# Optimization experiments

Hardware: AMD Instinct MI355X
Metric: run time of the kernel (lower is better)

Reference implementation:

```python
import jax, jax.numpy as jnp
import numpy as np

M = 0.25
GAMMA = 256.0
HARD_W = 2.0
O_P = 1.0 + M
O_N = -M
DELTA_P = 1.0 - M
DELTA_N = M
NEG_BIG = -1e30  # masked-out fill for logsumexp (finite to keep grads NaN-free)


def setup_inputs() -> dict:
    key = jax.random.key(0)
    k1, k2 = jax.random.split(key)
    inputs = jax.random.normal(k1, (4096, 512), dtype=jnp.float32)
    targets = jax.random.randint(k2, (4096,), 0, 64, dtype=jnp.int64)
    return {"inputs": inputs, "targets": targets}


def reference(inputs, targets):
    n = inputs.shape[0]
    x = inputs / jnp.linalg.norm(inputs, axis=1, keepdims=True)  # L2 normalize
    sim = x @ x.T                                                # [n, n]

    same = targets[:, None] == targets[None, :]
    eye = jnp.eye(n, dtype=bool)
    pos_mask = same & ~eye
    neg_mask = ~same
    npos = pos_mask.sum(axis=1)
    nneg = neg_mask.sum(axis=1)

    sim_d = jax.lax.stop_gradient(sim)  # alphas are detached in the original
    alpha_p = jax.nn.relu(O_P - sim_d)
    alpha_n = jax.nn.relu(sim_d - O_N)

    # hard mining: scale alpha at hardest positive (min sim) / hardest negative (max sim)
    idx = jnp.arange(n)
    hard_p = jnp.argmin(jnp.where(pos_mask, sim_d, jnp.inf), axis=1)
    hard_n = jnp.argmax(jnp.where(neg_mask, sim_d, -jnp.inf), axis=1)
    hit_p = (idx[None, :] == hard_p[:, None]) & (npos > 1)[:, None]
    hit_n = (idx[None, :] == hard_n[:, None]) & (nneg > 1)[:, None]
    alpha_p = alpha_p * jnp.where(hit_p, HARD_W, 1.0)
    alpha_n = alpha_n * jnp.where(hit_n, HARD_W, 1.0)

    pos_term = jnp.where(pos_mask, -GAMMA * alpha_p * (sim - DELTA_P), NEG_BIG)
    neg_term = jnp.where(neg_mask, GAMMA * alpha_n * (sim - DELTA_N), NEG_BIG)
    lse_p = jax.nn.logsumexp(pos_term, axis=1)
    lse_n = jax.nn.logsumexp(neg_term, axis=1)

    valid = (npos > 0) & (nneg > 0)
    per_row = jnp.where(valid, jax.nn.softplus(lse_p + lse_n), 0.0)
    n_valid = jnp.maximum(valid.sum(), 1)
    return per_row.sum() / n_valid.astype(per_row.dtype)
```

## Files before the change

### kernel.cpp

```cpp
#include <hip/hip_runtime.h>


#define MASKT_  (-1.0e4f)
#define MINITP_ (-1.0e4f)
#define MASKP_  (-3.0e4f)
#define QA_     369.3299304675f
#define QB_     (-23.08312065422f)
#define LN2_    0.6931471805599453f

constexpr int N_ = 4096;
constexpr int D_ = 512;
constexpr int AST_ = 520;
constexpr int CCH_ = 16;

typedef __bf16 bf16x8 __attribute__((ext_vector_type(8)));
typedef float  f32x4  __attribute__((ext_vector_type(4)));
typedef const unsigned int __attribute__((address_space(1)))* gp_t;
typedef unsigned int       __attribute__((address_space(3)))* lp_t;

__device__ __forceinline__ float pos_q(float s) {
    float d = s - 1.0f;
    return fmaf(d * d, 256.0f, -16.0f);
}
__device__ __forceinline__ float neg_q(float s) {
    float q = fmaf(s * s, 256.0f, -16.0f);
    return (s >= -0.25f) ? q : 0.0f;
}
__device__ __forceinline__ float neg_q2(float s) {
    float q = fmaf(s * s, QA_, QB_);
    return (s >= -0.25f) ? q : 0.0f;
}
__device__ __forceinline__ void lse_merge(float m2, float S2, float& m, float& S) {
    float mm = fmaxf(m, m2);
    S = S * __expf(m - mm) + S2 * __expf(m2 - mm);
    m = mm;
}
__device__ __forceinline__ void lse_merge2(float m2, float S2, float& m, float& S) {
    float mm = fmaxf(m, m2);
    S = S * exp2f(m - mm) + S2 * exp2f(m2 - mm);
    m = mm;
}
__device__ __forceinline__ unsigned short f2bf(float f) {
    unsigned int u = __float_as_uint(f);
    unsigned int r = u + 0x7FFFu + ((u >> 16) & 1u);
    return (unsigned short)(r >> 16);
}

__global__ __launch_bounds__(256) void k_norm(const float* __restrict__ in,
                                              unsigned short* __restrict__ xb,
                                              float* __restrict__ acc) {
    const int row  = blockIdx.x * 4 + (threadIdx.x >> 6);
    const int lane = threadIdx.x & 63;
    const float4* src = (const float4*)(in + (size_t)row * D_) + lane * 2;
    float4 a = src[0], b = src[1];
    float ss = a.x*a.x + a.y*a.y + a.z*a.z + a.w*a.w
             + b.x*b.x + b.y*b.y + b.z*b.z + b.w*b.w;
    #pragma unroll
    for (int d = 32; d >= 1; d >>= 1) ss += __shfl_xor(ss, d);
    float rn = 1.0f / sqrtf(ss);
    float v[8] = {a.x, a.y, a.z, a.w, b.x, b.y, b.z, b.w};
    union { uint4 u; unsigned short us[8]; } pk;
    #pragma unroll
    for (int k = 0; k < 8; ++k) pk.us[k] = f2bf(v[k] * rn);
    *((uint4*)(xb + (size_t)row * D_) + lane) = pk.u;
    if (blockIdx.x == 0 && threadIdx.x < 4) acc[threadIdx.x] = 0.0f;
}

__global__ __launch_bounds__(256, 4) void k_mainW(const unsigned short* __restrict__ xb,
                                                  const int* __restrict__ tg,
                                                  float* __restrict__ part) {
    constexpr int NST = 16;
    __shared__ __align__(16) unsigned short Bs[2][16][AST_];

    {
        const int ph = ((int)blockIdx.x >> 8) & 3;
        if (ph == 1)      __builtin_amdgcn_s_sleep(7);
        else if (ph == 2) __builtin_amdgcn_s_sleep(14);
        else if (ph == 3) __builtin_amdgcn_s_sleep(21);
    }

    const int tid  = threadIdx.x;
    const int wave = tid >> 6, lane = tid & 63;
    const int n16  = lane & 15, quad = lane >> 4;
    const int rg   = (int)blockIdx.x >> 4;
    const int cc   = (int)blockIdx.x & 15;
    const int rowBase = rg * 64 + wave * 16;
    const int colBase = cc * 256;

    bf16x8 af[16];
    {
        const bf16x8* ap = (const bf16x8*)(xb + (size_t)(rowBase + n16) * D_ + quad * 8);
        #pragma unroll
        for (int kk = 0; kk < 16; ++kk) af[kk] = ap[kk * 4];
    }
    int tr[4];
    #pragma unroll
    for (int r = 0; r < 4; ++r) tr[r] = tg[rowBase + quad * 4 + r];

    float m_p[4], S_p[4], S_n[4], mxn[4];
    #pragma unroll
    for (int r = 0; r < 4; ++r) {
        m_p[r] = MINITP_; S_p[r] = 0.f; S_n[r] = 0.f; mxn[r] = -2.0f;
    }

    const char* gstage = (const char*)xb + (size_t)colBase * 1024 + lane * 16;

    asm volatile("s_waitcnt vmcnt(0)" ::: "memory");

    #pragma unroll
    for (int p = 0; p < 4; ++p) {
        int j = p * 4 + wave;
        __builtin_amdgcn_global_load_lds((gp_t)(const void*)(gstage + j * 1024),
                                         (lp_t)(void*)&Bs[0][j][0], 16, 0, 0);
    }
    int tc_cur = tg[colBase + n16];

    auto epi = [&](const f32x4& a0, const f32x4& a1, int tcv, bool withDiag) {
        #pragma unroll
        for (int r = 0; r < 4; ++r) {
            float sim = a0[r] + a1[r];
            bool samec = (tr[r] == tcv);
            float dm1 = sim - 1.0f;
            float tp  = fmaf(dm1 * dm1, QA_, QB_);
            tp = samec ? tp : MASKP_;
            if (withDiag && n16 == quad * 4 + r) tp = MASKP_;
            float diff = m_p[r] - tp;
            float e    = exp2f(-fabsf(diff));
            float sA   = S_p[r] + e;
            float sB   = fmaf(S_p[r], e, 1.0f);
            S_p[r] = (diff < 0.0f) ? sB : sA;
            m_p[r] = fmaxf(m_p[r], tp);
            float tn = fmaf(sim * sim, QA_, QB_);
            float en = exp2f(tn);
            en = (sim >= -0.25f) ? en : 1.0f;
            en = samec ? 0.0f : en;
            S_n[r] += en;
            mxn[r] = fmaxf(mxn[r], samec ? -2.0f : sim);
        }
    };

    #pragma unroll 1
    for (int u = 0; u < NST; ++u) {
        const int b = u & 1;
        const int j0 = colBase + u * 16;

        int tc_nxt = 0;
        if (u + 1 < NST) {
            const char* g2 = gstage + (size_t)(u + 1) * 16384;
            #pragma unroll
            for (int p = 0; p < 4; ++p) {
                int j = p * 4 + wave;
                __builtin_amdgcn_global_load_lds((gp_t)(const void*)(g2 + j * 1024),
                                                 (lp_t)(void*)&Bs[b ^ 1][j][0], 16, 0, 0);
            }
            tc_nxt = tg[colBase + (u + 1) * 16 + n16];
            asm volatile("s_waitcnt vmcnt(5)" ::: "memory");
        } else {
            asm volatile("s_waitcnt vmcnt(0)" ::: "memory");
        }
        __builtin_amdgcn_s_barrier();
        __builtin_amdgcn_sched_barrier(0);

        f32x4 a0 = {0.f, 0.f, 0.f, 0.f}, a1 = {0.f, 0.f, 0.f, 0.f};
        __builtin_amdgcn_s_setprio(1);
        #pragma unroll
        for (int kk = 0; kk < 8; ++kk) {
            bf16x8 bf0 = *(const bf16x8*)&Bs[b][n16][(2 * kk) * 32 + quad * 8];
            bf16x8 bf1 = *(const bf16x8*)&Bs[b][n16][(2 * kk + 1) * 32 + quad * 8];
            a0 = __builtin_amdgcn_mfma_f32_16x16x32_bf16(af[2 * kk],     bf0, a0, 0, 0, 0);
            a1 = __builtin_amdgcn_mfma_f32_16x16x32_bf16(af[2 * kk + 1], bf1, a1, 0, 0, 0);
        }
        __builtin_amdgcn_s_setprio(0);

        if (j0 == rowBase) epi(a0, a1, tc_cur, true);
        else               epi(a0, a1, tc_cur, false);
        tc_cur = tc_nxt;

        if (u + 1 < NST) __builtin_amdgcn_s_barrier();
    }

    #pragma unroll
    for (int r = 0; r < 4; ++r) {
        #pragma unroll
        for (int d = 1; d <= 8; d <<= 1) {
            lse_merge2(__shfl_xor(m_p[r], d), __shfl_xor(S_p[r], d), m_p[r], S_p[r]);
            S_n[r] += __shfl_xor(S_n[r], d);
            mxn[r] = fmaxf(mxn[r], __shfl_xor(mxn[r], d));
        }
    }
    if (n16 == 0) {
        #pragma unroll
        for (int r = 0; r < 4; ++r) {
            ((float4*)part)[(size_t)(rowBase + quad * 4 + r) * CCH_ + cc] =
                make_float4(m_p[r], S_p[r], mxn[r], S_n[r]);
        }
    }
}

__global__ __launch_bounds__(256) void k_reduceF(const float* __restrict__ part,
                                                 const int* __restrict__ tg,
                                                 float* __restrict__ acc,
                                                 float* __restrict__ out) {
    __shared__ int hist[64];
    const int tid = threadIdx.x;
    if (tid < 64) hist[tid] = 0;
    __syncthreads();
    for (int i = tid; i < N_; i += 256) atomicAdd(&hist[tg[i]], 1);
    __syncthreads();

    const int row = blockIdx.x * 256 + tid;
    const float4* P = (const float4*)part + (size_t)row * CCH_;
    float M_p = MINITP_, Sp = 0.f, M_n = 0.f, Sn = 0.f, mxn = -2.0f;
    #pragma unroll
    for (int c = 0; c < CCH_; ++c) {
        float4 a = P[c];
        lse_merge2(a.x, a.y, M_p, Sp);
        Sn += a.w;
        mxn = fmaxf(mxn, a.z);
    }
    const int cnt = hist[tg[row]];
    float np2 = (float)(cnt - 1), nn2 = (float)(N_ - cnt);
    float loss = 0.f, vld = 0.f;
    if (np2 > 0.5f && nn2 > 0.5f) {
        if (np2 > 1.5f) {
            float t1 = M_p, t2 = 2.0f * t1;
            float mm = fmaxf(M_p, t2);
            Sp = Sp * exp2f(M_p - mm) + exp2f(t2 - mm) - exp2f(t1 - mm);
            M_p = mm;
        }
        if (nn2 > 1.5f) {
            float t1 = neg_q2(mxn), t2 = 2.0f * t1;
            float mm = fmaxf(M_n, t2);
            Sn = Sn * exp2f(M_n - mm) + exp2f(t2 - mm) - exp2f(t1 - mm);
            M_n = mm;
        }
        float z = LN2_ * ((M_p + __log2f(Sp)) + (M_n + __log2f(Sn)));
        loss = fmaxf(z, 0.0f) + log1pf(__expf(-fabsf(z)));
        vld = 1.0f;
    }
    #pragma unroll
    for (int d = 32; d >= 1; d >>= 1) { loss += __shfl_xor(loss, d); vld += __shfl_xor(vld, d); }
    if ((tid & 63) == 0) { atomicAdd(&acc[0], loss); atomicAdd(&acc[1], vld); }

    __syncthreads();
    if (tid == 0) {
        __threadfence();
        int old = atomicAdd((int*)(acc + 2), 1);
        if (old == (int)gridDim.x - 1) {
            float ls = atomicAdd(&acc[0], 0.0f);
            float lv = atomicAdd(&acc[1], 0.0f);
            out[0] = ls / fmaxf(lv, 1.0f);
        }
    }
}

__global__ void k_final(const float* __restrict__ acc, float* __restrict__ out) {
    if (threadIdx.x == 0) out[0] = acc[0] / fmaxf(acc[1], 1.0f);
}

__global__ void k_sentinel(float* __restrict__ out) {
    if (threadIdx.x == 0) out[0] = -12345.0f;
}

__global__ __launch_bounds__(1024, 4) void k_main3(const unsigned short* __restrict__ xb,
                                                   const int* __restrict__ tg,
                                                   float* __restrict__ acc_g) {
    __shared__ __align__(16) unsigned short As[16 * AST_];
    __shared__ float sm[16][16][8];
    const int tid  = threadIdx.x;
    const int wave = tid >> 6, lane = tid & 63;
    const int n16  = lane & 15, quad = lane >> 4;
    const int rowBase = blockIdx.x * 16;
    {
        int row = tid >> 6, c = tid & 63;
        *(uint4*)&As[row * AST_ + c * 8] =
            *(const uint4*)(xb + (size_t)(rowBase + row) * D_ + c * 8);
    }
    int ir[4], tr[4];
    #pragma unroll
    for (int r = 0; r < 4; ++r) { ir[r] = rowBase + quad * 4 + r; tr[r] = tg[ir[r]]; }
    float m_p[4], S_p[4], m_n[4], S_n[4], mnp[4], mxn[4], sc[4];
    #pragma unroll
    for (int r = 0; r < 4; ++r) {
        m_p[r] = 0.f; S_p[r] = 0.f; m_n[r] = 0.f; S_n[r] = 0.f;
        mnp[r] = 2.0f; mxn[r] = -2.0f; sc[r] = 0.f;
    }
    __syncthreads();
    const unsigned short* Af = &As[n16 * AST_ + quad * 8];
    #pragma unroll 1
    for (int t = wave; t < N_ / 16; t += 16) {
        const int jcol = t * 16 + n16;
        const int tc = tg[jcol];
        const bf16x8* bp = (const bf16x8*)(xb + (size_t)jcol * D_ + quad * 8);
        bf16x8 bf[16];
        #pragma unroll
        for (int kk = 0; kk < 16; ++kk) bf[kk] = bp[kk * 4];
        f32x4 a0 = {0.f, 0.f, 0.f, 0.f}, a1 = {0.f, 0.f, 0.f, 0.f};
        #pragma unroll
        for (int kk = 0; kk < 8; ++kk) {
            bf16x8 af0 = *(const bf16x8*)(Af + (2 * kk) * 32);
            bf16x8 af1 = *(const bf16x8*)(Af + (2 * kk + 1) * 32);
            a0 = __builtin_amdgcn_mfma_f32_16x16x32_bf16(af0, bf[2 * kk],     a0, 0, 0, 0);
            a1 = __builtin_amdgcn_mfma_f32_16x16x32_bf16(af1, bf[2 * kk + 1], a1, 0, 0, 0);
        }
        #pragma unroll
        for (int r = 0; r < 4; ++r) {
            float s = a0[r] + a1[r];
            bool samec = (tr[r] == tc);
            bool posm  = samec && (jcol != ir[r]);
            float tp = posm  ? pos_q(s) : MASKT_;
            float tn = samec ? MASKT_ : neg_q(s);
            float mm = fmaxf(m_p[r], tp);
            S_p[r] = S_p[r] * __expf(m_p[r] - mm) + __expf(tp - mm); m_p[r] = mm;
            mm = fmaxf(m_n[r], tn);
            S_n[r] = S_n[r] * __expf(m_n[r] - mm) + __expf(tn - mm); m_n[r] = mm;
            sc[r] += samec ? 1.0f : 0.0f;
            mnp[r] = fminf(mnp[r], posm ? s : 2.0f);
            mxn[r] = fmaxf(mxn[r], samec ? -2.0f : s);
        }
    }
    #pragma unroll
    for (int r = 0; r < 4; ++r) {
        #pragma unroll
        for (int d = 1; d <= 8; d <<= 1) {
            lse_merge(__shfl_xor(m_p[r], d), __shfl_xor(S_p[r], d), m_p[r], S_p[r]);
            lse_merge(__shfl_xor(m_n[r], d), __shfl_xor(S_n[r], d), m_n[r], S_n[r]);
            mnp[r] = fminf(mnp[r], __shfl_xor(mnp[r], d));
            mxn[r] = fmaxf(mxn[r], __shfl_xor(mxn[r], d));
            sc[r] += __shfl_xor(sc[r], d);
        }
    }
    if (n16 == 0) {
        #pragma unroll
        for (int r = 0; r < 4; ++r) {
            float* q = sm[wave][quad * 4 + r];
            q[0] = m_p[r]; q[1] = S_p[r]; q[2] = m_n[r]; q[3] = S_n[r];
            q[4] = mnp[r]; q[5] = mxn[r]; q[6] = sc[r];
        }
    }
    __syncthreads();
    if (tid < 64) {
        const int L = tid & 15;
        float m_p2 = 0.f, S_p2 = 0.f, m_n2 = 0.f, S_n2 = 0.f;
        float mnp2 = 2.0f, mxn2 = -2.0f, sct = 0.f;
        #pragma unroll
        for (int w = 0; w < 16; ++w) {
            const float* q = sm[w][L];
            lse_merge(q[0], q[1], m_p2, S_p2);
            lse_merge(q[2], q[3], m_n2, S_n2);
            mnp2 = fminf(mnp2, q[4]); mxn2 = fmaxf(mxn2, q[5]);
            sct += q[6];
        }
        float loss = 0.f, vld = 0.f;
        float np2 = sct - 1.0f, nn2 = (float)N_ - sct;
        if (tid < 16 && np2 > 0.5f && nn2 > 0.5f) {
            if (np2 > 1.5f) {
                float t1 = pos_q(mnp2), t2 = 2.0f * t1;
                float mm = fmaxf(m_p2, t2);
                S_p2 = S_p2 * __expf(m_p2 - mm) + __expf(t2 - mm) - __expf(t1 - mm);
                m_p2 = mm;
            }
            if (nn2 > 1.5f) {
                float t1 = neg_q(mxn2), t2 = 2.0f * t1;
                float mm = fmaxf(m_n2, t2);
                S_n2 = S_n2 * __expf(m_n2 - mm) + __expf(t2 - mm) - __expf(t1 - mm);
                m_n2 = mm;
            }
            float z = (m_p2 + __logf(S_p2)) + (m_n2 + __logf(S_n2));
            loss = fmaxf(z, 0.0f) + log1pf(__expf(-fabsf(z)));
            vld = 1.0f;
        }
        #pragma unroll
        for (int d = 32; d >= 1; d >>= 1) {
            loss += __shfl_xor(loss, d); vld += __shfl_xor(vld, d);
        }
        if (tid == 0) { atomicAdd(&acc_g[0], loss); atomicAdd(&acc_g[1], vld); }
    }
}

extern "C" void kernel_launch(void* const* d_in, const int* in_sizes, int n_in,
                              void* d_out, int out_size, void* d_ws, size_t ws_size,
                              hipStream_t stream) {
    const float* in = (const float*)d_in[0];
    const int*   tg = (const int*)d_in[1];
    constexpr size_t MB = 1024 * 1024;
    unsigned short* xb = (unsigned short*)d_ws;

    if (ws_size >= 5 * MB + 64) {
        float* part = (float*)((char*)d_ws + 4 * MB);
        float* acc  = (float*)((char*)d_ws + 5 * MB);
        hipLaunchKernelGGL(k_norm,    dim3(N_ / 4),    dim3(256), 0, stream, in, xb, acc);
        hipLaunchKernelGGL(k_mainW,   dim3(64 * CCH_), dim3(256), 0, stream, xb, tg, part);
        hipLaunchKernelGGL(k_reduceF, dim3(N_ / 256),  dim3(256), 0, stream, part, tg, acc,
                           (float*)d_out);
    } else if (ws_size >= 4 * MB + 64) {
        float* acc = (float*)((char*)d_ws + 4 * MB);
        hipLaunchKernelGGL(k_norm,  dim3(N_ / 4),  dim3(256),  0, stream, in, xb, acc);
        hipLaunchKernelGGL(k_main3, dim3(N_ / 16), dim3(1024), 0, stream, xb, tg, acc);
        hipLaunchKernelGGL(k_final, dim3(1),       dim3(64),   0, stream, acc, (float*)d_out);
    } else {
        hipLaunchKernelGGL(k_sentinel, dim3(1), dim3(64), 0, stream, (float*)d_out);
    }
}
```

Measured before the change: 107.1 us.

## Fuse norm, main and reduce kernels into one cooperative grid-synced kernel

Merges the three launches (normalize, similarity/LSE tiles, final reduce) into a single cooperative kernel of 1024 blocks that separates the phases with grid-wide syncs. The aim is to remove two kernel launch gaps and the associated drain/refill overhead. The cost is two grid barriers, and the kernel needs all 1024 blocks co-resident at 4 per CU. It falls back to the three-kernel path if the cooperative launch fails.

```diff
diff --git a/kernel.cpp b/kernel.cpp
--- a/kernel.cpp
+++ b/kernel.cpp
@@ -1,4 +1,7 @@
 #include <hip/hip_runtime.h>
+#include <hip/hip_cooperative_groups.h>
+
+namespace cg = cooperative_groups;
 
 
 #define MASKT_  (-1.0e4f)
@@ -44,6 +47,216 @@
     unsigned int u = __float_as_uint(f);
     unsigned int r = u + 0x7FFFu + ((u >> 16) & 1u);
     return (unsigned short)(r >> 16);
+}
+
+__global__ __launch_bounds__(256, 4) void k_fusedX(const float* __restrict__ in,
+                                                   const int* __restrict__ tg,
+                                                   unsigned short* __restrict__ xb,
+                                                   float* __restrict__ part,
+                                                   float* __restrict__ acc,
+                                                   float* __restrict__ out) {
+    constexpr int NST = 16;
+    __shared__ __align__(16) unsigned short Bs[2][16][AST_];
+    __shared__ int hist[64];
+
+    const int b    = (int)blockIdx.x;
+    const int tid  = threadIdx.x;
+    const int wave = tid >> 6, lane = tid & 63;
+    const int n16  = lane & 15, quad = lane >> 4;
+
+    {
+        const int row = b * 4 + wave;
+        const float4* src = (const float4*)(in + (size_t)row * D_) + lane * 2;
+        float4 a = src[0], c = src[1];
+        float ss = a.x*a.x + a.y*a.y + a.z*a.z + a.w*a.w
+                 + c.x*c.x + c.y*c.y + c.z*c.z + c.w*c.w;
+        #pragma unroll
+        for (int d = 32; d >= 1; d >>= 1) ss += __shfl_xor(ss, d);
+        float rn = 1.0f / sqrtf(ss);
+        float v[8] = {a.x, a.y, a.z, a.w, c.x, c.y, c.z, c.w};
+        union { uint4 u; unsigned short us[8]; } pk;
+        #pragma unroll
+        for (int k = 0; k < 8; ++k) pk.us[k] = f2bf(v[k] * rn);
+        *((uint4*)(xb + (size_t)row * D_) + lane) = pk.u;
+        if (b == 0 && tid < 4) acc[tid] = 0.0f;
+    }
+    cg::this_grid().sync();
+
+    {
+        const int ph = (b >> 8) & 3;
+        if (ph == 1)      __builtin_amdgcn_s_sleep(7);
+        else if (ph == 2) __builtin_amdgcn_s_sleep(14);
+        else if (ph == 3) __builtin_amdgcn_s_sleep(21);
+
+        const int rg = b >> 4;
+        const int cc = b & 15;
+        const int rowBase = rg * 64 + wave * 16;
+        const int colBase = cc * 256;
+
+        bf16x8 af[16];
+        {
+            const bf16x8* ap = (const bf16x8*)(xb + (size_t)(rowBase + n16) * D_ + quad * 8);
+            #pragma unroll
+            for (int kk = 0; kk < 16; ++kk) af[kk] = ap[kk * 4];
+        }
+        int tr[4];
+        #pragma unroll
+        for (int r = 0; r < 4; ++r) tr[r] = tg[rowBase + quad * 4 + r];
+
+        float m_p[4], S_p[4], S_n[4], mxn[4];
+        #pragma unroll
+        for (int r = 0; r < 4; ++r) {
+            m_p[r] = MINITP_; S_p[r] = 0.f; S_n[r] = 0.f; mxn[r] = -2.0f;
+        }
+
+        const char* gstage = (const char*)xb + (size_t)colBase * 1024 + lane * 16;
+
+        asm volatile("s_waitcnt vmcnt(0)" ::: "memory");
+
+        #pragma unroll
+        for (int p = 0; p < 4; ++p) {
+            int j = p * 4 + wave;
+            __builtin_amdgcn_global_load_lds((gp_t)(const void*)(gstage + j * 1024),
+                                             (lp_t)(void*)&Bs[0][j][0], 16, 0, 0);
+        }
+        int tc_cur = tg[colBase + n16];
+
+        auto epi = [&](const f32x4& a0, const f32x4& a1, int tcv, bool withDiag) {
+            #pragma unroll
+            for (int r = 0; r < 4; ++r) {
+                float sim = a0[r] + a1[r];
+                bool samec = (tr[r] == tcv);
+                float dm1 = sim - 1.0f;
+                float tp  = fmaf(dm1 * dm1, QA_, QB_);
+                tp = samec ? tp : MASKP_;
+                if (withDiag && n16 == quad * 4 + r) tp = MASKP_;
+                float diff = m_p[r] - tp;
+                float e    = exp2f(-fabsf(diff));
+                float sA   = S_p[r] + e;
+                float sB   = fmaf(S_p[r], e, 1.0f);
+                S_p[r] = (diff < 0.0f) ? sB : sA;
+                m_p[r] = fmaxf(m_p[r], tp);
+                float tn = fmaf(sim * sim, QA_, QB_);
+                float en = exp2f(tn);
+                en = (sim >= -0.25f) ? en : 1.0f;
+                en = samec ? 0.0f : en;
+                S_n[r] += en;
+                mxn[r] = fmaxf(mxn[r], samec ? -2.0f : sim);
+            }
+        };
+
+        #pragma unroll 1
+        for (int u = 0; u < NST; ++u) {
+            const int bb = u & 1;
+            const int j0 = colBase + u * 16;
+
+            int tc_nxt = 0;
+            if (u + 1 < NST) {
+                const char* g2 = gstage + (size_t)(u + 1) * 16384;
+                #pragma unroll
+                for (int p = 0; p < 4; ++p) {
+                    int j = p * 4 + wave;
+                    __builtin_amdgcn_global_load_lds((gp_t)(const void*)(g2 + j * 1024),
+                                                     (lp_t)(void*)&Bs[bb ^ 1][j][0], 16, 0, 0);
+                }
+                tc_nxt = tg[colBase + (u + 1) * 16 + n16];
+                asm volatile("s_waitcnt vmcnt(5)" ::: "memory");
+            } else {
+                asm volatile("s_waitcnt vmcnt(0)" ::: "memory");
+            }
+            __builtin_amdgcn_s_barrier();
+            __builtin_amdgcn_sched_barrier(0);
+
+            f32x4 a0 = {0.f, 0.f, 0.f, 0.f}, a1 = {0.f, 0.f, 0.f, 0.f};
+            __builtin_amdgcn_s_setprio(1);
+            #pragma unroll
+            for (int kk = 0; kk < 8; ++kk) {
+                bf16x8 bf0 = *(const bf16x8*)&Bs[bb][n16][(2 * kk) * 32 + quad * 8];
+                bf16x8 bf1 = *(const bf16x8*)&Bs[bb][n16][(2 * kk + 1) * 32 + quad * 8];
+                a0 = __builtin_amdgcn_mfma_f32_16x16x32_bf16(af[2 * kk],     bf0, a0, 0, 0, 0);
+                a1 = __builtin_amdgcn_mfma_f32_16x16x32_bf16(af[2 * kk + 1], bf1, a1, 0, 0, 0);
+            }
+            __builtin_amdgcn_s_setprio(0);
+
+            if (j0 == rowBase) epi(a0, a1, tc_cur, true);
+            else               epi(a0, a1, tc_cur, false);
+            tc_cur = tc_nxt;
+
+            if (u + 1 < NST) __builtin_amdgcn_s_barrier();
+        }
+
+        #pragma unroll
+        for (int r = 0; r < 4; ++r) {
+            #pragma unroll
+            for (int d = 1; d <= 8; d <<= 1) {
+                lse_merge2(__shfl_xor(m_p[r], d), __shfl_xor(S_p[r], d), m_p[r], S_p[r]);
+                S_n[r] += __shfl_xor(S_n[r], d);
+                mxn[r] = fmaxf(mxn[r], __shfl_xor(mxn[r], d));
+            }
+        }
+        if (n16 == 0) {
+            #pragma unroll
+            for (int r = 0; r < 4; ++r) {
+                ((float4*)part)[(size_t)(rowBase + quad * 4 + r) * CCH_ + cc] =
+                    make_float4(m_p[r], S_p[r], mxn[r], S_n[r]);
+            }
+        }
+    }
+    cg::this_grid().sync();
+
+    if (b < 16) {
+        if (tid < 64) hist[tid] = 0;
+        __syncthreads();
+        for (int i = tid; i < N_; i += 256) atomicAdd(&hist[tg[i]], 1);
+        __syncthreads();
+
+        const int row = b * 256 + tid;
+        const float4* P = (const float4*)part + (size_t)row * CCH_;
+        float M_p = MINITP_, Sp = 0.f, M_n = 0.f, Sn = 0.f, mxn = -2.0f;
+        #pragma unroll
+        for (int c = 0; c < CCH_; ++c) {
+            float4 a = P[c];
+            lse_merge2(a.x, a.y, M_p, Sp);
+            Sn += a.w;
+            mxn = fmaxf(mxn, a.z);
+        }
+        const int cnt = hist[tg[row]];
+        float np2 = (float)(cnt - 1), nn2 = (float)(N_ - cnt);
+        float loss = 0.f, vld = 0.f;
+        if (np2 > 0.5f && nn2 > 0.5f) {
+            if (np2 > 1.5f) {
+                float t1 = M_p, t2 = 2.0f * t1;
+                float mm = fmaxf(M_p, t2);
+                Sp = Sp * exp2f(M_p - mm) + exp2f(t2 - mm) - exp2f(t1 - mm);
+                M_p = mm;
+            }
+            if (nn2 > 1.5f) {
+                float t1 = neg_q2(mxn), t2 = 2.0f * t1;
+                float mm = fmaxf(M_n, t2);
+                Sn = Sn * exp2f(M_n - mm) + exp2f(t2 - mm) - exp2f(t1 - mm);
+                M_n = mm;
+            }
+            float z = LN2_ * ((M_p + __log2f(Sp)) + (M_n + __log2f(Sn)));
+            loss = fmaxf(z, 0.0f) + log1pf(__expf(-fabsf(z)));
+            vld = 1.0f;
+        }
+        #pragma unroll
+        for (int d = 32; d >= 1; d >>= 1) {
+            loss += __shfl_xor(loss, d); vld += __shfl_xor(vld, d);
+        }
+        if ((tid & 63) == 0) { atomicAdd(&acc[0], loss); atomicAdd(&acc[1], vld); }
+
+        __syncthreads();
+        if (tid == 0) {
+            __threadfence();
+            int old = atomicAdd((int*)(acc + 2), 1);
+            if (old == 16 - 1) {
+                float ls = atomicAdd(&acc[0], 0.0f);
+                float lv = atomicAdd(&acc[1], 0.0f);
+                out[0] = ls / fmaxf(lv, 1.0f);
+            }
+        }
+    }
 }
 
 __global__ __launch_bounds__(256) void k_norm(const float* __restrict__ in,
@@ -71,14 +284,12 @@
                                                   float* __restrict__ part) {
     constexpr int NST = 16;
     __shared__ __align__(16) unsigned short Bs[2][16][AST_];
-
     {
         const int ph = ((int)blockIdx.x >> 8) & 3;
         if (ph == 1)      __builtin_amdgcn_s_sleep(7);
         else if (ph == 2) __builtin_amdgcn_s_sleep(14);
         else if (ph == 3) __builtin_amdgcn_s_sleep(21);
     }
-
     const int tid  = threadIdx.x;
     const int wave = tid >> 6, lane = tid & 63;
     const int n16  = lane & 15, quad = lane >> 4;
@@ -102,11 +313,8 @@
     for (int r = 0; r < 4; ++r) {
         m_p[r] = MINITP_; S_p[r] = 0.f; S_n[r] = 0.f; mxn[r] = -2.0f;
     }
-
     const char* gstage = (const char*)xb + (size_t)colBase * 1024 + lane * 16;
-
     asm volatile("s_waitcnt vmcnt(0)" ::: "memory");
-
     #pragma unroll
     for (int p = 0; p < 4; ++p) {
         int j = p * 4 + wave;
@@ -143,7 +351,6 @@
     for (int u = 0; u < NST; ++u) {
         const int b = u & 1;
         const int j0 = colBase + u * 16;
-
         int tc_nxt = 0;
         if (u + 1 < NST) {
             const char* g2 = gstage + (size_t)(u + 1) * 16384;
@@ -175,7 +382,6 @@
         if (j0 == rowBase) epi(a0, a1, tc_cur, true);
         else               epi(a0, a1, tc_cur, false);
         tc_cur = tc_nxt;
-
         if (u + 1 < NST) __builtin_amdgcn_s_barrier();
     }
 
@@ -389,10 +595,18 @@
     if (ws_size >= 5 * MB + 64) {
         float* part = (float*)((char*)d_ws + 4 * MB);
         float* acc  = (float*)((char*)d_ws + 5 * MB);
-        hipLaunchKernelGGL(k_norm,    dim3(N_ / 4),    dim3(256), 0, stream, in, xb, acc);
-        hipLaunchKernelGGL(k_mainW,   dim3(64 * CCH_), dim3(256), 0, stream, xb, tg, part);
-        hipLaunchKernelGGL(k_reduceF, dim3(N_ / 256),  dim3(256), 0, stream, part, tg, acc,
-                           (float*)d_out);
+        float* outp = (float*)d_out;
+
+        void* ka[] = { (void*)&in, (void*)&tg, (void*)&xb,
+                       (void*)&part, (void*)&acc, (void*)&outp };
+        hipError_t e = hipLaunchCooperativeKernel((const void*)k_fusedX,
+                                                  dim3(1024), dim3(256), ka, 0, stream);
+        if (e != hipSuccess) {
+            hipLaunchKernelGGL(k_norm,    dim3(N_ / 4),    dim3(256), 0, stream, in, xb, acc);
+            hipLaunchKernelGGL(k_mainW,   dim3(64 * CCH_), dim3(256), 0, stream, xb, tg, part);
+            hipLaunchKernelGGL(k_reduceF, dim3(N_ / 256),  dim3(256), 0, stream, part, tg,
+                               acc, outp);
+        }
     } else if (ws_size >= 4 * MB + 64) {
         float* acc = (float*)((char*)d_ws + 4 * MB);
         hipLaunchKernelGGL(k_norm,  dim3(N_ / 4),  dim3(256),  0, stream, in, xb, acc);
```

Result: slower. 286.2 us (+167.1%).
